# Kernel optimization log

Hardware: AMD Instinct MI355X
Metric: run time of the kernel (lower is better)

The kernel has to match this reference:

```python
import jax, jax.numpy as jnp
import numpy as np
from jax import lax

B, T, D, H = 64, 2048, 128, 256  # batch, seq_len, input_dim, hidden_dim


def setup_inputs() -> dict:
    key = jax.random.key(0)
    ks = jax.random.split(key, 21)
    s = 0.05
    p = lambda k, shape: jax.random.normal(k, shape, dtype=jnp.float32) * s
    inp = {"x": jax.random.normal(ks[0], (B, T, D), dtype=jnp.float32)}
    i = 1
    for n in ["e1", "e2", "d1", "d2"]:  # encode1, encode2, reconstruct1, reconstruct2
        inp[n + "_Wih"] = p(ks[i], (4 * H, D)); i += 1
        inp[n + "_Whh"] = p(ks[i], (4 * H, H)); i += 1
        inp[n + "_bih"] = p(ks[i], (4 * H,)); i += 1
        inp[n + "_bhh"] = p(ks[i], (4 * H,)); i += 1
    inp["l1_W"] = p(ks[17], (D, H)); inp["l1_b"] = p(ks[18], (D,))
    inp["l2_W"] = p(ks[19], (D, H)); inp["l2_b"] = p(ks[20], (D,))
    return inp


def _lstm_cell(h, c, xt, Wih, Whh, bih, bhh):
    # PyTorch gate order: i, f, g, o
    g = xt @ Wih.T + h @ Whh.T + bih + bhh  # [B, 4H]
    i, f, gg, o = jnp.split(g, 4, axis=-1)
    c = jax.nn.sigmoid(f) * c + jax.nn.sigmoid(i) * jnp.tanh(gg)
    h = jax.nn.sigmoid(o) * jnp.tanh(c)
    return h, c


def _encode(x, h0, c0, Wih, Whh, bih, bhh):
    # x: [B, T, D] batch_first -> scan over time
    def step(carry, xt):
        h, c = carry
        h, c = _lstm_cell(h, c, xt, Wih, Whh, bih, bhh)
        return (h, c), None
    (h, c), _ = lax.scan(step, (h0, c0), jnp.swapaxes(x, 0, 1))
    return h, c


def _decode(n, h, c, Wih, Whh, bih, bhh, Wl, bl):
    # first output is linear(hidden) before any cell step (matches original decode)
    inp0 = h @ Wl.T + bl  # [B, D]
    def step(carry, _):
        h, c, inp = carry
        h, c = _lstm_cell(h, c, inp, Wih, Whh, bih, bhh)
        inp = h @ Wl.T + bl
        return (h, c, inp), inp
    _, outs = lax.scan(step, (h, c, inp0), None, length=n - 1)  # [n-1, B, D]
    out = jnp.concatenate([inp0[None], outs], axis=0)  # [n, B, D]
    return jnp.swapaxes(out, 0, 1)  # [B, n, D]


def reference(x,
              e1_Wih, e1_Whh, e1_bih, e1_bhh,
              e2_Wih, e2_Whh, e2_bih, e2_bhh,
              d1_Wih, d1_Whh, d1_bih, d1_bhh,
              d2_Wih, d2_Whh, d2_bih, d2_bhh,
              l1_W, l1_b, l2_W, l2_b):
    Bc, Tc = x.shape[0], x.shape[1]
    T1 = Tc // 2
    h0 = jnp.zeros((Bc, H), dtype=x.dtype)
    c0 = jnp.zeros((Bc, H), dtype=x.dtype)
    x1 = x[:, :T1][:, ::-1]  # first half, time-reversed
    x2 = x[:, T1:]
    h1, c1 = _encode(x1, h0, c0, e1_Wih, e1_Whh, e1_bih, e1_bhh)
    h2, c2 = _encode(x2, h1, c1, e2_Wih, e2_Whh, e2_bih, e2_bhh)
    out1 = _decode(T1, h1, c1, d1_Wih, d1_Whh, d1_bih, d1_bhh, l1_W, l1_b)
    out2 = _decode(Tc - T1, h2, c2, d2_Wih, d2_Whh, d2_bih, d2_bhh, l2_W, l2_b)[:, ::-1]
    return jnp.concatenate([out1, out2], axis=1)  # [B, T, D]
```

## Files before the change

### kernel.cpp

```cpp
#include <hip/hip_runtime.h>
#include <stdint.h>

#define Bv 64
#define Tv 2048
#define T1v 1024
#define Dv 128
#define Hv 256

typedef _Float16 h2_t __attribute__((ext_vector_type(2)));
typedef _Float16 f16x8 __attribute__((ext_vector_type(8)));
typedef float f32x4 __attribute__((ext_vector_type(4)));

__device__ inline float d2(uint32_t hp, uint32_t wp, float acc) {
#if __has_builtin(__builtin_amdgcn_fdot2)
  return __builtin_amdgcn_fdot2(__builtin_bit_cast(h2_t, hp),
                                __builtin_bit_cast(h2_t, wp), acc, false);
#else
  float out;
  asm("v_dot2_f32_f16 %0, %1, %2, %3" : "=v"(out) : "v"(hp), "v"(wp), "v"(acc));
  return out;
#endif
}

__device__ inline uint16_t f2h(float x) {
// ... 25 lines not shown
  const float2* x2 = (const float2*)x;
  float2 v = x2[idx];
  xpk[idx] = packpair(v.x, v.y);
}

__global__ void k_pack_w(const float* __restrict__ src, uint32_t* __restrict__ wAll,
                         uint32_t* __restrict__ wLg, uint32_t* __restrict__ wStr) {
  int idx = blockIdx.x * 256 + threadIdx.x;
  int row = idx >> 7, k2 = idx & 127;
  uint32_t pr = packpair(src[row * 256 + 2 * k2], src[row * 256 + 2 * k2 + 1]);
  wAll[k2 * 1024 + row] = pr;
  if (k2 >= 96) {
    int g = (k2 - 96) >> 2, qq = (k2 - 96) & 3;
    wLg[(g * 1024 + row) * 4 + qq] = pr;
  }
  if (k2 >= 48 && k2 < 96) wStr[row * 48 + (k2 - 48)] = pr;
}

__global__ void k_pack_w2(const float* __restrict__ src, uint32_t* __restrict__ wReg,
                          uint32_t* __restrict__ wLds) {
  int idx = blockIdx.x * 256 + threadIdx.x;
  int r = idx >> 7, k2 = idx & 127;
  uint32_t pr = packpair(src[r * 256 + 2 * k2], src[r * 256 + 2 * k2 + 1]);
  int gate = r >> 8, u = r & 255;
  int u_hi = u >> 7, jb = u & 127;
  int q = k2 >> 5, kk = k2 & 31;
  int tid = jb * 4 + q;
  int ri = u_hi * 4 + gate;
  int cc = kk >> 2, c = kk & 3;
  if (cc < 6) wReg[((ri * 6 + cc) * 512 + tid) * 4 + c] = pr;
  else        wLds[((ri * 2 + (cc - 6)) * 512 + tid) * 4 + c] = pr;
}

__global__ void k_pack_wf(const float* __restrict__ src, uint32_t* __restrict__ resF,
                          uint32_t* __restrict__ ldsF, uint32_t* __restrict__ strF,
                          int CR, int CL, int CS) {
  int idx = blockIdx.x * 256 + threadIdx.x;
  int r = idx >> 7, k2 = idx & 127;
  int k = 2 * k2;
  uint32_t pr = packpair(src[r * 256 + k], src[r * 256 + k + 1]);
  int gate = r >> 8, u = r & 255;
  int rowp = u * 4 + gate;
  int t = rowp >> 4, w = t >> 3, tt = t & 7, rr = rowp & 15;
  int c = k >> 5, kk = k & 31;
  int lane = rr + 16 * (kk >> 3);
  int dw = (kk & 7) >> 1;
  if (c < CR) {
    resF[(((w * CR + c) * 8 + tt) * 64 + lane) * 4 + dw] = pr;
  } else if (c < CR + CL) {
    ldsF[(((w * CL + (c - CR)) * 8 + tt) * 64 + lane) * 4 + dw] = pr;
  } else {
    int cs = c - CR - CL;
    size_t o = (((size_t)(w * CS + cs) * 8 + tt) * 64 + lane) * 4 + dw;
    strF[o] = pr;
    strF[o + (size_t)CS * 4096 * 4] = pr;
  }
}

__global__ void k_pack_biasf(const float* __restrict__ b32, uint16_t* __restrict__ biasF) {
  int r = blockIdx.x * 256 + threadIdx.x;
  if (r >= 1024) return;
  int gate = r >> 8, u = r & 255;
  int rowp = u * 4 + gate;
  int t = rowp >> 4, w = t >> 3, tt = t & 7, rr = rowp & 15;
  int lg = rr >> 2, reg = rr & 3;
  uint16_t v = f2h(b32[r]);
  for (int bl = 0; bl < 16; ++bl)
    biasF[(w * 64 + (bl + 16 * lg)) * 32 + tt * 4 + reg] = v;
}

__global__ void k_bias_pack(const float* __restrict__ b32, uint32_t* __restrict__ bpk) {
  int jb = threadIdx.x;
  uint32_t w[4];
#pragma unroll
  for (int wi = 0; wi < 4; ++wi) {
    int ri0 = 2 * wi, ri1 = 2 * wi + 1;
    int row0 = (ri0 & 3) * 256 + jb + 128 * (ri0 >> 2);
    int row1 = (ri1 & 3) * 256 + jb + 128 * (ri1 >> 2);
    w[wi] = packpair(b32[row0], b32[row1]);
  }
  ((uint4*)bpk)[jb] = make_uint4(w[0], w[1], w[2], w[3]);
}

__global__ void k_pack_wih(const float* __restrict__ Wih, uint32_t* __restrict__ wihp) {
  int idx = blockIdx.x * 256 + threadIdx.x;
  int row = idx >> 6, k2 = idx & 63;
  wihp[row * 64 + k2] = packpair(Wih[row * 128 + 2 * k2], Wih[row * 128 + 2 * k2 + 1]);
}

__global__ void k_bias2(const float* __restrict__ bih, const float* __restrict__ bhh,
                        float* __restrict__ bias) {
  int i = blockIdx.x * 256 + threadIdx.x;
  if (i < 1024) bias[i] = bih[i] + bhh[i];
}

__global__ void k_dec_combine(const float* __restrict__ Whh, const float* __restrict__ Wih,
                              const float* __restrict__ bih, const float* __restrict__ bhh,
                              const float* __restrict__ lW, const float* __restrict__ lb,
                              float* __restrict__ wd, float* __restrict__ bias) {
  int j = blockIdx.x;
  int k = threadIdx.x;
  __shared__ float wr[128];
  if (k < 128) wr[k] = Wih[j * 128 + k];
  __syncthreads();
  float acc = Whh[j * 256 + k];
  for (int d = 0; d < 128; ++d) acc += wr[d] * lW[d * 256 + k];
  wd[j * 256 + k] = acc;
  if (k == 0) {
    float s = bih[j] + bhh[j];
    for (int d = 0; d < 128; ++d) s += wr[d] * lb[d];
    bias[j] = s;
  }
}

__global__ void k_pack_wl(const float* __restrict__ lW, uint32_t* __restrict__ wlp) {
  int idx = blockIdx.x * 256 + threadIdx.x;
  int d = idx >> 7, k2 = idx & 127;
  wlp[d * 128 + k2] = packpair(lW[d * 256 + 2 * k2], lW[d * 256 + 2 * k2 + 1]);
}

template <int LAY>
__global__ __launch_bounds__(256) void k_xp_gemm(const uint32_t* __restrict__ xpk,
                                                 const uint32_t* __restrict__ wihp,
                                                 uint16_t* __restrict__ xp, int xt0, int xdt) {
  const int b = blockIdx.z;
  const int s0 = blockIdx.y * 32;
  const int r = blockIdx.x * 256 + threadIdx.x;
  uint32_t wreg[64];
#pragma unroll
  for (int k = 0; k < 64; ++k) wreg[k] = wihp[r * 64 + k];
  const int gate = r >> 8, u = r & 255;
  const int u_hi = u >> 7, jb = u & 127;
  const int ri = u_hi * 4 + gate;
  for (int sl = 0; sl < 32; ++sl) {
    const int s = s0 + sl;
    const int t = xt0 + s * xdt;
    const uint32_t* __restrict__ xrow = xpk + ((size_t)b * Tv + t) * 64;
    float a0 = 0.f, a1 = 0.f;
#pragma unroll
    for (int k = 0; k < 64; k += 2) {
      a0 = d2(xrow[k], wreg[k], a0);
      a1 = d2(xrow[k + 1], wreg[k + 1], a1);
    }
    uint16_t v = f2h(a0 + a1);
    if (LAY == 0)
      xp[(((size_t)b * T1v + s) * 128 + jb) * 8 + ri] = v;
    else
      xp[((size_t)b * T1v + s) * 1024 + r] = v;
  }
}

__global__ __launch_bounds__(256) void k_xp_gemmF(const uint32_t* __restrict__ xpk,
                                                  const uint32_t* __restrict__ wihp,
                                                  const float* __restrict__ bias,
                                                  uint16_t* __restrict__ xpf, int xt0, int xdt) {
  const int b = blockIdx.z;
  const int s0 = blockIdx.y * 32;
  const int r = blockIdx.x * 256 + threadIdx.x;
  uint32_t wreg[64];
#pragma unroll
  for (int k = 0; k < 64; ++k) wreg[k] = wihp[r * 64 + k];
  const float bv = bias[r];
  const int gate = r >> 8, u = r & 255;
  const int rowp = u * 4 + gate;
  const int t = rowp >> 4, w = t >> 3, tt = t & 7, rr = rowp & 15;
  const int lane = (b & 15) + 16 * (rr >> 2);
  const int reg = rr & 3;
  const int bt = b >> 4;
  for (int sl = 0; sl < 32; ++sl) {
    const int s = s0 + sl;
    const int tx = xt0 + s * xdt;
    const uint32_t* __restrict__ xrow = xpk + ((size_t)b * Tv + tx) * 64;
    float a0 = 0.f, a1 = 0.f;
#pragma unroll
    for (int k = 0; k < 64; k += 2) {
      a0 = d2(xrow[k], wreg[k], a0);
      a1 = d2(xrow[k + 1], wreg[k + 1], a1);
    }
    xpf[(((size_t)bt * 1024 + s) * 512 + w * 64 + lane) * 32 + tt * 4 + reg] =
        f2h(a0 + a1 + bv);
  }
}


struct CfgM {
  const uint4* resF;
  const uint4* ldsF;
  const uint4* strF;
  const uint16_t* biasF;
  const uint16_t* xpf;
  const float* h0;
  const float* c0;
  float* hN;
  float* cN;
  uint16_t* hist;
};

template <int CR, int CL, int CS>
__global__ void __launch_bounds__(512)
__attribute__((amdgpu_waves_per_eu(2, 2)))
k_rnnM(CfgM cA, CfgM cB, int nA) {
  __shared__ __align__(16) uint4 wldsA[CL > 0 ? CL * 4096 : 1];
  __shared__ __align__(16) uint16_t hb[2][16][264];

  const bool isA = (int)blockIdx.x < nA;
  const CfgM cfg = isA ? cA : cB;
  const int bi = isA ? (int)blockIdx.x : ((int)blockIdx.x - nA);
  const int b0 = bi * 16;
  const int tid = threadIdx.x;
  const int w = tid >> 6, l = tid & 63;
  const int bl = l & 15, lg = l >> 4;

  if (CL > 0) {
#pragma unroll
    for (int i = 0; i < CL * 8; ++i) wldsA[i * 512 + tid] = cfg.ldsF[i * 512 + tid];
  }

  uint4 wrA[CR * 8];
#pragma unroll
  for (int i = 0; i < CR * 8; ++i) wrA[i] = cfg.resF[((size_t)w * CR * 8 + i) * 64 + l];

  uint4 bh[4];
#pragma unroll
  for (int j = 0; j < 4; ++j) bh[j] = ((const uint4*)cfg.biasF)[(w * 64 + l) * 4 + j];

  float cst[8];
#pragma unroll
  for (int tt = 0; tt < 8; ++tt) {
    int unit = (w * 8 + tt) * 4 + lg;
    cst[tt] = cfg.c0 ? cfg.c0[(b0 + bl) * 256 + unit] : 0.f;
  }

  {
    int batch = tid >> 5, u0 = (tid & 31) * 8;
    uint16_t tmp[8];
#pragma unroll
    for (int j = 0; j < 8; ++j)
      tmp[j] = f2h(cfg.h0 ? cfg.h0[(b0 + batch) * 256 + u0 + j] : 0.f);
    *(uint4*)((char*)&hb[0][0][0] + batch * 528 + u0 * 2) = *(const uint4*)tmp;
  }
  __syncthreads();

  char* hb0 = (char*)&hb[0][0][0];
  const size_t hbsz = 16 * 264 * 2;
  int cur = 0;

  for (int s = 0; s < 1024; ++s) {
    const char* hbc = hb0 + (size_t)cur * hbsz;

    if (cfg.hist) {
      int batch = tid >> 5, u0 = (tid & 31) * 8;
      uint4 hv = *(const uint4*)(hbc + batch * 528 + u0 * 2);
      *(uint4*)(cfg.hist + ((size_t)(b0 + batch) * 1024 + s) * 256 + u0) = hv;
    }

    f32x4 acc[8];
    if (cfg.xpf) {
      const uint4* xp4 = (const uint4*)(cfg.xpf + (((size_t)bi * 1024 + s) * 512 + tid) * 32);
      uint4 xh[4];
#pragma unroll
      for (int j = 0; j < 4; ++j) xh[j] = xp4[j];
      const _Float16* xv = (const _Float16*)xh;
#pragma unroll
      for (int tt = 0; tt < 8; ++tt)
#pragma unroll
        for (int rg = 0; rg < 4; ++rg) acc[tt][rg] = (float)xv[tt * 4 + rg];
    } else {
      const _Float16* bv = (const _Float16*)bh;
#pragma unroll
      for (int tt = 0; tt < 8; ++tt)
#pragma unroll
        for (int rg = 0; rg < 4; ++rg) acc[tt][rg] = (float)bv[tt * 4 + rg];
    }

#pragma unroll
    for (int c = 0; c < CR; ++c) {
      f16x8 bf = __builtin_bit_cast(f16x8,
          *(const uint4*)(hbc + bl * 528 + c * 64 + lg * 16));
#pragma unroll
      for (int tt = 0; tt < 8; ++tt)
        acc[tt] = __builtin_amdgcn_mfma_f32_16x16x32_f16(
            __builtin_bit_cast(f16x8, wrA[c * 8 + tt]), bf, acc[tt], 0, 0, 0);
    }
    if (CL > 0) {
#pragma unroll
      for (int cl = 0; cl < CL; ++cl) {
        const int c = CR + cl;
        f16x8 bf = __builtin_bit_cast(f16x8,
            *(const uint4*)(hbc + bl * 528 + c * 64 + lg * 16));
#pragma unroll
        for (int tt = 0; tt < 8; ++tt) {
          uint4 au = wldsA[(w * CL + cl) * 512 + tt * 64 + l];
          acc[tt] = __builtin_amdgcn_mfma_f32_16x16x32_f16(
              __builtin_bit_cast(f16x8, au), bf, acc[tt], 0, 0, 0);
        }
      }
    }
    if (CS > 0) {
      const uint4* sp = cfg.strF + ((s & 1) ? (size_t)CS * 4096 : 0);
      uint4 pf[8];
#pragma unroll
      for (int tt = 0; tt < 8; ++tt) pf[tt] = sp[((size_t)w * CS) * 512 + tt * 64 + l];
#pragma unroll
      for (int cs = 0; cs < CS; ++cs) {
        const int c = CR + CL + cs;
        uint4 cu[8];
#pragma unroll
        for (int tt = 0; tt < 8; ++tt) cu[tt] = pf[tt];
        if (cs + 1 < CS) {
#pragma unroll
          for (int tt = 0; tt < 8; ++tt)
            pf[tt] = sp[((size_t)w * CS + cs + 1) * 512 + tt * 64 + l];
        }
        f16x8 bf = __builtin_bit_cast(f16x8,
            *(const uint4*)(hbc + bl * 528 + c * 64 + lg * 16));
#pragma unroll
        for (int tt = 0; tt < 8; ++tt)
          acc[tt] = __builtin_amdgcn_mfma_f32_16x16x32_f16(
              __builtin_bit_cast(f16x8, cu[tt]), bf, acc[tt], 0, 0, 0);
      }
    }

    char* hbn = hb0 + (size_t)(cur ^ 1) * hbsz;
#pragma unroll
    for (int tt = 0; tt < 8; ++tt) {
      const float i_ = sigm(acc[tt][0]);
      const float f_ = sigm(acc[tt][1]);
      const float g_ = tanh_(acc[tt][2]);
      const float o_ = sigm(acc[tt][3]);
      const float cn = f_ * cst[tt] + i_ * g_;
      cst[tt] = cn;
      const float hv = o_ * tanh_(cn);
      const int unit = (w * 8 + tt) * 4 + lg;
      *(uint16_t*)(hbn + bl * 528 + unit * 2) = f2h(hv);
    }
    __syncthreads();
    cur ^= 1;
  }

  if (cfg.hN) {
    const char* hbc = hb0 + (size_t)cur * hbsz;
    int batch = tid >> 5, u0 = (tid & 31) * 8;
#pragma unroll
    for (int j = 0; j < 8; ++j)
      cfg.hN[(b0 + batch) * 256 + u0 + j] =
          h2f(*(const uint16_t*)(hbc + batch * 528 + (u0 + j) * 2));
#pragma unroll
    for (int tt = 0; tt < 8; ++tt) {
      int unit = (w * 8 + tt) * 4 + lg;
      cfg.cN[(b0 + bl) * 256 + unit] = cst[tt];
    }
  }
}


struct CfgU {
  const uint4* wA;
  const uint4* wC;
  const uint4* bpk;
  const uint4* xps;
  const float* h0;
  const float* c0;
  float* hN;
  float* cN;
  uint16_t* hist;
};

__global__ void __launch_bounds__(512)
__attribute__((amdgpu_waves_per_eu(2, 2)))
k_rnnU6(CfgU cA, CfgU cB, int nA) {
  __shared__ __align__(16) uint4 wldsM[2 * 8 * 512];
  __shared__ __align__(16) uint16_t hbuf[2][4][72];

  const bool isA = (int)blockIdx.x < nA;
  const CfgU cfg = isA ? cA : cB;
  const int b = isA ? (int)blockIdx.x : ((int)blockIdx.x - nA);
  const int tid = threadIdx.x;
  const int q = tid & 3, jb = tid >> 2;

#pragma unroll
  for (int i = 0; i < 16; ++i) wldsM[i * 512 + tid] = cfg.wC[i * 512 + tid];

  uint4 wr[8][6];
#pragma unroll
  for (int ri = 0; ri < 8; ++ri)
#pragma unroll
    for (int cc = 0; cc < 6; ++cc) wr[ri][cc] = cfg.wA[(ri * 6 + cc) * 512 + tid];

  const uint4 bp = cfg.bpk[jb];
  float c0r = cfg.c0 ? cfg.c0[b * 256 + jb] : 0.f;
  float c1r = cfg.c0 ? cfg.c0[b * 256 + jb + 128] : 0.f;

  uint16_t* histp = cfg.hist ? cfg.hist + (size_t)b * 1024 * 256 : nullptr;
  if (q == 0) {
    float h00 = cfg.h0 ? cfg.h0[b * 256 + jb] : 0.f;
    float h01 = cfg.h0 ? cfg.h0[b * 256 + jb + 128] : 0.f;
    uint16_t u0 = f2h(h00), u1 = f2h(h01);
    hbuf[0][jb >> 6][jb & 63] = u0;
    hbuf[0][2 + (jb >> 6)][jb & 63] = u1;
    if (histp) {
      histp[jb] = u0;
      histp[jb + 128] = u1;
    }
  }
  const uint4* xps4 = cfg.xps ? cfg.xps + (size_t)b * 1024 * 128 + jb : nullptr;

  __syncthreads();

  int cur = 0;
  for (int s = 0; s < 1024; ++s) {
    uint4 xq = make_uint4(0, 0, 0, 0);
    if (xps4) xq = xps4[(size_t)s * 128];
    const uint4* Hq = (const uint4*)(&hbuf[cur][q][0]);

    float acc[8];
#pragma unroll
    for (int ri = 0; ri < 8; ++ri) acc[ri] = 0.f;

#pragma unroll
    for (int cc = 0; cc < 6; ++cc) {
      const uint4 hv = Hq[cc];
#pragma unroll
      for (int ri = 0; ri < 8; ++ri) {
        acc[ri] = d2(hv.x, wr[ri][cc].x, acc[ri]);
        acc[ri] = d2(hv.y, wr[ri][cc].y, acc[ri]);
        acc[ri] = d2(hv.z, wr[ri][cc].z, acc[ri]);
        acc[ri] = d2(hv.w, wr[ri][cc].w, acc[ri]);
      }
    }
#pragma unroll
    for (int lI = 0; lI < 2; ++lI) {
      const uint4 hv = Hq[6 + lI];
#pragma unroll
      for (int ri = 0; ri < 8; ++ri) {
        const uint4 wv = wldsM[(ri * 2 + lI) * 512 + tid];
        acc[ri] = d2(hv.x, wv.x, acc[ri]);
        acc[ri] = d2(hv.y, wv.y, acc[ri]);
        acc[ri] = d2(hv.z, wv.z, acc[ri]);
        acc[ri] = d2(hv.w, wv.w, acc[ri]);
      }
    }

#pragma unroll
    for (int ri = 0; ri < 8; ++ri) acc[ri] = qsum4(acc[ri]);

    acc[0] += unpk(bp.x, 0) + unpk(xq.x, 0);
    acc[1] += unpk(bp.x, 1) + unpk(xq.x, 1);
    acc[2] += unpk(bp.y, 0) + unpk(xq.y, 0);
    acc[3] += unpk(bp.y, 1) + unpk(xq.y, 1);
    acc[4] += unpk(bp.z, 0) + unpk(xq.z, 0);
    acc[5] += unpk(bp.z, 1) + unpk(xq.z, 1);
    acc[6] += unpk(bp.w, 0) + unpk(xq.w, 0);
    acc[7] += unpk(bp.w, 1) + unpk(xq.w, 1);

    const float cn0 = sigm(acc[1]) * c0r + sigm(acc[0]) * tanh_(acc[2]);
    const float h0v = sigm(acc[3]) * tanh_(cn0);
    c0r = cn0;
    const float cn1 = sigm(acc[5]) * c1r + sigm(acc[4]) * tanh_(acc[6]);
    const float h1v = sigm(acc[7]) * tanh_(cn1);
    c1r = cn1;

    if (q == 0) {
      const uint16_t hu0 = f2h(h0v), hu1 = f2h(h1v);
      hbuf[cur ^ 1][jb >> 6][jb & 63] = hu0;
      hbuf[cur ^ 1][2 + (jb >> 6)][jb & 63] = hu1;
      if (histp && s < 1023) {
        histp[(size_t)(s + 1) * 256 + jb] = hu0;
        histp[(size_t)(s + 1) * 256 + jb + 128] = hu1;
      }
    }
    __syncthreads();
    cur ^= 1;
  }

  if (cfg.hN && q == 0) {
    cfg.hN[b * 256 + jb] = h2f(hbuf[cur][jb >> 6][jb & 63]);
    cfg.hN[b * 256 + jb + 128] = h2f(hbuf[cur][2 + (jb >> 6)][jb & 63]);
    cfg.cN[b * 256 + jb] = c0r;
    cfg.cN[b * 256 + jb + 128] = c1r;
  }
}


struct ChainCfg {
  const uint32_t* wAll;
  const uint4* wLg;
  const uint32_t* wStr;
// ... 107 lines not shown
    for (int g = 0; g < 8; ++g) {
      const uint4 hv = H4[24 + g];
      const uint4 wv0 = wlds4[g * 1024 + r0];
      const uint4 wv1 = wlds4[g * 1024 + r1];
      a00 = d2(hv.x, wv0.x, a00);
      a01 = d2(hv.y, wv0.y, a01);
      a10 = d2(hv.x, wv1.x, a10);
      a11 = d2(hv.y, wv1.y, a11);
      a00 = d2(hv.z, wv0.z, a00);
      a01 = d2(hv.w, wv0.w, a01);
      a10 = d2(hv.z, wv1.z, a10);
      a11 = d2(hv.w, wv1.w, a11);
    }
    if constexpr (WIH) {
      if (cfg.wih) {
        const uint4* XS4 = (const uint4*)xsh;
#pragma unroll
        for (int u = 0; u < 16; ++u) {
          const uint4 xv = XS4[u];
          const uint4 wv0 = wi0[u];
          const uint4 wv1 = wi1[u];
          a00 = d2(xv.x, wv0.x, a00);
          a01 = d2(xv.y, wv0.y, a01);
          a10 = d2(xv.x, wv1.x, a10);
          a11 = d2(xv.y, wv1.y, a11);
          a00 = d2(xv.z, wv0.z, a00);
          a01 = d2(xv.w, wv0.w, a01);
          a10 = d2(xv.z, wv1.z, a10);
          a11 = d2(xv.w, wv1.w, a11);
        }
      }
    }

    gsm[r0] = a00 + a01 + xa0;
    gsm[r1] = a10 + a11 + xa1;
    __syncthreads();

    if (tid < 256) {
      const float gi = gsm[tid];
      const float gf = gsm[tid + 256];
      const float gg = gsm[tid + 512];
      const float go = gsm[tid + 768];
      const float cn = sigm(gf) * creg + sigm(gi) * tanh_(gg);
      const float hv = sigm(go) * tanh_(cn);
      creg = cn;
      const uint16_t hu = f2h(hv);
      h16[tid] = hu;
      if (histp && s < 1023) histp[(size_t)(s + 1) * 256 + tid] = hu;
    }
    __syncthreads();
  }

  if (cfg.hN && tid < 256) {
    cfg.hN[b * 256 + tid] = h2f(h16[tid]);
    cfg.cN[b * 256 + tid] = creg;
  }
}

__global__ __launch_bounds__(256) void k_out(const uint16_t* __restrict__ hist,
                                             const uint32_t* __restrict__ wlp,
                                             const float* __restrict__ lb,
                                             float* __restrict__ out, int outbase, int tsign) {
  const int b = blockIdx.y;
  const int t0 = blockIdx.x * 64;
  __shared__ __align__(16) uint32_t hq[64 * 128];
  const uint32_t* hsrc = (const uint32_t*)hist;
  for (int i = threadIdx.x; i < 64 * 128; i += 256) {
    hq[i] = hsrc[((size_t)b * 1024 + t0) * 128 + i];
  }
  __syncthreads();
  const int d = threadIdx.x & 127;
  const int th = threadIdx.x >> 7;
  float acc[32];
#pragma unroll
  for (int it = 0; it < 32; ++it) acc[it] = lb[d];
  const uint4* W4 = (const uint4*)(wlp + (size_t)d * 128);
  const uint4* HQ4 = (const uint4*)hq;
  for (int k2c = 0; k2c < 32; ++k2c) {
    const uint4 wv = W4[k2c];
#pragma unroll
    for (int it = 0; it < 32; ++it) {
      const int tl = th * 32 + it;
      const uint4 hv = HQ4[tl * 32 + k2c];
      acc[it] = d2(hv.x, wv.x, acc[it]);
      acc[it] = d2(hv.y, wv.y, acc[it]);
      acc[it] = d2(hv.z, wv.z, acc[it]);
      acc[it] = d2(hv.w, wv.w, acc[it]);
    }
  }
#pragma unroll
  for (int it = 0; it < 32; ++it) {
    const int tl = th * 32 + it;
    const int t = t0 + tl;
    const int tout = outbase + tsign * t;
    out[((size_t)b * Tv + tout) * Dv + d] = acc[it];
  }
}


extern "C" void kernel_launch(void* const* d_in, const int* in_sizes, int n_in,
                              void* d_out, int out_size, void* d_ws, size_t ws_size,
                              hipStream_t stream) {
  const float* x = (const float*)d_in[0];
  const float* e1_Wih = (const float*)d_in[1];
  const float* e1_Whh = (const float*)d_in[2];
  const float* e1_bih = (const float*)d_in[3];
  const float* e1_bhh = (const float*)d_in[4];
  const float* e2_Wih = (const float*)d_in[5];
  const float* e2_Whh = (const float*)d_in[6];
  const float* e2_bih = (const float*)d_in[7];
  const float* e2_bhh = (const float*)d_in[8];
  const float* d1_Wih = (const float*)d_in[9];
  const float* d1_Whh = (const float*)d_in[10];
  const float* d1_bih = (const float*)d_in[11];
  const float* d1_bhh = (const float*)d_in[12];
  const float* d2_Wih = (const float*)d_in[13];
  const float* d2_Whh = (const float*)d_in[14];
  const float* d2_bih = (const float*)d_in[15];
  const float* d2_bhh = (const float*)d_in[16];
  const float* l1_W = (const float*)d_in[17];
  const float* l1_b = (const float*)d_in[18];
  const float* l2_W = (const float*)d_in[19];
  const float* l2_b = (const float*)d_in[20];

  uint8_t* wsb = (uint8_t*)d_ws;
  size_t off = 0;
  auto take = [&](size_t n) -> void* {
    void* pp = wsb + off;
    off += (n + 255) & ~(size_t)255;
    return pp;
  };
  uint32_t* xpk = (uint32_t*)take((size_t)Bv * Tv * 64 * 4);
  uint16_t* hist1 = (uint16_t*)take((size_t)Bv * T1v * Hv * 2);
  uint16_t* hist2 = (uint16_t*)take((size_t)Bv * T1v * Hv * 2);
  struct WSet {
    uint32_t *wAll, *wLg, *wStr48, *wih;
    float* bias;
    uint32_t *wReg, *wLds, *bpk;
    uint32_t *resF, *ldsF, *strF;
    uint16_t* biasF;
  };
  auto take_wset = [&](bool with_ih) -> WSet {
    WSet w;
    w.wAll = (uint32_t*)take(128 * 1024 * 4);
    w.wLg = (uint32_t*)take(8 * 1024 * 16);
    w.wStr48 = (uint32_t*)take(1024 * 48 * 4);
    w.wih = with_ih ? (uint32_t*)take(1024 * 64 * 4) : nullptr;
    w.bias = (float*)take(1024 * 4);
    w.wReg = (uint32_t*)take(48 * 512 * 16);
    w.wLds = (uint32_t*)take(16 * 512 * 16);
    w.bpk = (uint32_t*)take(128 * 16);
    w.resF = (uint32_t*)take((size_t)5 * 4096 * 16);
    w.ldsF = (uint32_t*)take((size_t)2 * 4096 * 16);
    w.strF = (uint32_t*)take((size_t)2 * 3 * 4096 * 16);
    w.biasF = (uint16_t*)take(512 * 32 * 2);
    return w;
  };
  WSet we1 = take_wset(true);
  WSet we2 = take_wset(true);
  WSet wd1 = take_wset(false);
  WSet wd2 = take_wset(false);
  float* wd32 = (float*)take(1024 * 256 * 4);
  uint32_t* wl1p = (uint32_t*)take(128 * 128 * 4);
  uint32_t* wl2p = (uint32_t*)take(128 * 128 * 4);
  float* h1 = (float*)take(64 * 256 * 4);
  float* c1 = (float*)take(64 * 256 * 4);
  float* h2 = (float*)take(64 * 256 * 4);
  float* c2 = (float*)take(64 * 256 * 4);
  uint16_t* xp = (uint16_t*)take((size_t)Bv * T1v * 1024 * 2);
  const bool use_xp = ws_size >= off;

  int variant = 5;
  int MCR = 0, MCL = 0, MCS = 0;
  {
    hipFuncAttributes fa;
    auto sf = [&](const void* f) {
      return hipFuncGetAttributes(&fa, f) == hipSuccess && fa.localSizeBytes == 0;
    };
    if (use_xp) {
      if (sf(reinterpret_cast<const void*>(&k_rnnM<5, 1, 2>))) { variant = 0; MCR = 5; MCL = 1; MCS = 2; }
      else if (sf(reinterpret_cast<const void*>(&k_rnnM<4, 2, 2>))) { variant = 1; MCR = 4; MCL = 2; MCS = 2; }
      else if (sf(reinterpret_cast<const void*>(&k_rnnM<3, 2, 3>))) { variant = 2; MCR = 3; MCL = 2; MCS = 3; }
      else if (sf(reinterpret_cast<const void*>(&k_rnnU6))) variant = 3;
      else if (sf(reinterpret_cast<const void*>(&k_rnn5<96, false>))) variant = 4;
    } else {
      if (sf(reinterpret_cast<const void*>(&k_rnn5<96, true>))) variant = 4;
    }
  }

  k_pack_x<<<(Bv * Tv * 64) / 256, 256, 0, stream>>>(x, xpk);
  k_pack_wih<<<256, 256, 0, stream>>>(e1_Wih, we1.wih);
  k_pack_wih<<<256, 256, 0, stream>>>(e2_Wih, we2.wih);
  k_bias2<<<4, 256, 0, stream>>>(e1_bih, e1_bhh, we1.bias);
  k_bias2<<<4, 256, 0, stream>>>(e2_bih, e2_bhh, we2.bias);
  k_pack_wl<<<64, 256, 0, stream>>>(l1_W, wl1p);
  k_pack_wl<<<64, 256, 0, stream>>>(l2_W, wl2p);

  if (variant <= 2) {
    k_pack_wf<<<512, 256, 0, stream>>>(e1_Whh, we1.resF, we1.ldsF, we1.strF, MCR, MCL, MCS);
    k_pack_wf<<<512, 256, 0, stream>>>(e2_Whh, we2.resF, we2.ldsF, we2.strF, MCR, MCL, MCS);
    k_pack_biasf<<<4, 256, 0, stream>>>(we1.bias, we1.biasF);
    k_pack_biasf<<<4, 256, 0, stream>>>(we2.bias, we2.biasF);
    k_dec_combine<<<1024, 256, 0, stream>>>(d1_Whh, d1_Wih, d1_bih, d1_bhh, l1_W, l1_b, wd32, wd1.bias);
    k_pack_wf<<<512, 256, 0, stream>>>(wd32, wd1.resF, wd1.ldsF, wd1.strF, MCR, MCL, MCS);
    k_pack_biasf<<<4, 256, 0, stream>>>(wd1.bias, wd1.biasF);
    k_dec_combine<<<1024, 256, 0, stream>>>(d2_Whh, d2_Wih, d2_bih, d2_bhh, l2_W, l2_b, wd32, wd2.bias);
    k_pack_wf<<<512, 256, 0, stream>>>(wd32, wd2.resF, wd2.ldsF, wd2.strF, MCR, MCL, MCS);
    k_pack_biasf<<<4, 256, 0, stream>>>(wd2.bias, wd2.biasF);

    auto mk = [&](WSet& w, const uint16_t* xpf, const float* h0, const float* c0,
                  float* hN, float* cN, uint16_t* hist) -> CfgM {
      return CfgM{(const uint4*)w.resF, (const uint4*)w.ldsF, (const uint4*)w.strF,
                  w.biasF, xpf, h0, c0, hN, cN, hist};
    };
    auto launch_m = [&](int grid, CfgM a, CfgM b2, int nA) {
      if (variant == 0)      k_rnnM<5, 1, 2><<<grid, 512, 0, stream>>>(a, b2, nA);
      else if (variant == 1) k_rnnM<4, 2, 2><<<grid, 512, 0, stream>>>(a, b2, nA);
      else                   k_rnnM<3, 2, 3><<<grid, 512, 0, stream>>>(a, b2, nA);
    };

    k_xp_gemmF<<<dim3(4, 32, 64), 256, 0, stream>>>(xpk, we1.wih, we1.bias, xp, 1023, -1);
    CfgM e1c = mk(we1, xp, nullptr, nullptr, h1, c1, nullptr);
    launch_m(4, e1c, e1c, 4);

    k_xp_gemmF<<<dim3(4, 32, 64), 256, 0, stream>>>(xpk, we2.wih, we2.bias, xp, 1024, 1);
    CfgM e2c = mk(we2, xp, h1, c1, h2, c2, nullptr);
    CfgM d1c = mk(wd1, nullptr, h1, c1, nullptr, nullptr, hist1);
    launch_m(8, e2c, d1c, 4);

    CfgM d2c = mk(wd2, nullptr, h2, c2, nullptr, nullptr, hist2);
    launch_m(4, d2c, d2c, 4);
  } else if (variant == 3) {
    k_pack_w2<<<512, 256, 0, stream>>>(e1_Whh, we1.wReg, we1.wLds);
    k_pack_w2<<<512, 256, 0, stream>>>(e2_Whh, we2.wReg, we2.wLds);
    k_bias_pack<<<1, 128, 0, stream>>>(we1.bias, we1.bpk);
    k_bias_pack<<<1, 128, 0, stream>>>(we2.bias, we2.bpk);
    k_dec_combine<<<1024, 256, 0, stream>>>(d1_Whh, d1_Wih, d1_bih, d1_bhh, l1_W, l1_b, wd32, wd1.bias);
    k_pack_w2<<<512, 256, 0, stream>>>(wd32, wd1.wReg, wd1.wLds);
    k_bias_pack<<<1, 128, 0, stream>>>(wd1.bias, wd1.bpk);
    k_dec_combine<<<1024, 256, 0, stream>>>(d2_Whh, d2_Wih, d2_bih, d2_bhh, l2_W, l2_b, wd32, wd2.bias);
    k_pack_w2<<<512, 256, 0, stream>>>(wd32, wd2.wReg, wd2.wLds);
    k_bias_pack<<<1, 128, 0, stream>>>(wd2.bias, wd2.bpk);

    auto mk = [&](WSet& w, const uint4* xps, const float* h0, const float* c0,
                  float* hN, float* cN, uint16_t* hist) -> CfgU {
      return CfgU{(const uint4*)w.wReg, (const uint4*)w.wLds,
                  (const uint4*)w.bpk, xps, h0, c0, hN, cN, hist};
    };
    k_xp_gemm<0><<<dim3(4, 32, 64), 256, 0, stream>>>(xpk, we1.wih, xp, 1023, -1);
    CfgU e1c = mk(we1, (const uint4*)xp, nullptr, nullptr, h1, c1, nullptr);
    k_rnnU6<<<64, 512, 0, stream>>>(e1c, e1c, 64);

    k_xp_gemm<0><<<dim3(4, 32, 64), 256, 0, stream>>>(xpk, we2.wih, xp, 1024, 1);
    CfgU e2c = mk(we2, (const uint4*)xp, h1, c1, h2, c2, nullptr);
    CfgU d1c = mk(wd1, nullptr, h1, c1, nullptr, nullptr, hist1);
    k_rnnU6<<<128, 512, 0, stream>>>(e2c, d1c, 64);

    CfgU d2c = mk(wd2, nullptr, h2, c2, nullptr, nullptr, hist2);
    k_rnnU6<<<64, 512, 0, stream>>>(d2c, d2c, 64);
  } else {
    k_pack_w<<<512, 256, 0, stream>>>(e1_Whh, we1.wAll, we1.wLg, we1.wStr48);
    k_pack_w<<<512, 256, 0, stream>>>(e2_Whh, we2.wAll, we2.wLg, we2.wStr48);
    k_dec_combine<<<1024, 256, 0, stream>>>(d1_Whh, d1_Wih, d1_bih, d1_bhh, l1_W, l1_b, wd32, wd1.bias);
    k_pack_w<<<512, 256, 0, stream>>>(wd32, wd1.wAll, wd1.wLg, wd1.wStr48);
    k_dec_combine<<<1024, 256, 0, stream>>>(d2_Whh, d2_Wih, d2_bih, d2_bhh, l2_W, l2_b, wd32, wd2.bias);
    k_pack_w<<<512, 256, 0, stream>>>(wd32, wd2.wAll, wd2.wLg, wd2.wStr48);

    auto launch_old = [&](int grid, ChainCfg a, ChainCfg b2, int nA) {
      if (use_xp) {
        if (variant == 4) k_rnn5<96, false><<<grid, 512, 0, stream>>>(a, b2, nA);
        else              k_rnn5<80, false><<<grid, 512, 0, stream>>>(a, b2, nA);
      } else {
        if (variant == 4) k_rnn5<96, true><<<grid, 512, 0, stream>>>(a, b2, nA);
        else              k_rnn5<80, true><<<grid, 512, 0, stream>>>(a, b2, nA);
      }
    };
    if (use_xp) k_xp_gemm<1><<<dim3(4, 32, 64), 256, 0, stream>>>(xpk, we1.wih, xp, 1023, -1);
    ChainCfg e1c{we1.wAll, (const uint4*)we1.wLg, we1.wStr48, use_xp ? nullptr : we1.wih,
                 use_xp ? nullptr : xpk, use_xp ? xp : nullptr, we1.bias,
                 nullptr, nullptr, h1, c1, nullptr, 1023, -1};
    launch_old(64, e1c, e1c, 64);

    if (use_xp) k_xp_gemm<1><<<dim3(4, 32, 64), 256, 0, stream>>>(xpk, we2.wih, xp, 1024, 1);
    ChainCfg e2c{we2.wAll, (const uint4*)we2.wLg, we2.wStr48, use_xp ? nullptr : we2.wih,
                 use_xp ? nullptr : xpk, use_xp ? xp : nullptr, we2.bias,
                 h1, c1, h2, c2, nullptr, 1024, 1};
    ChainCfg d1c{wd1.wAll, (const uint4*)wd1.wLg, wd1.wStr48, nullptr, nullptr, nullptr,
                 wd1.bias, h1, c1, nullptr, nullptr, hist1, 0, 0};
    launch_old(128, e2c, d1c, 64);

    ChainCfg d2c{wd2.wAll, (const uint4*)wd2.wLg, wd2.wStr48, nullptr, nullptr, nullptr,
                 wd2.bias, h2, c2, nullptr, nullptr, hist2, 0, 0};
    launch_old(64, d2c, d2c, 64);
  }

  k_out<<<dim3(16, 64), 256, 0, stream>>>(hist1, wl1p, l1_b, (float*)d_out, 0, 1);
  k_out<<<dim3(16, 64), 256, 0, stream>>>(hist2, wl2p, l2_b, (float*)d_out, 2047, -1);
}
```

Before: 7.167 ms.

## Rebalance Whh split to 5/2/1 and prefetch streamed weights before LDS chunks

Changes the recurrent weight split from 5 register, 1 LDS, 2 streamed chunks to 5/2/1, so less of Whh is streamed from global memory each timestep. The streamed-chunk load is issued at the top of the step, and the LDS chunks are computed between it and its use so the global latency is hidden. Bias and xp loads now share one strided pointer, which drops the per-thread bias registers. The 3/2/3 fallback variant is removed, and the LDS array is no longer guarded for CL=0.

```diff
diff --git a/kernel.cpp b/kernel.cpp
--- a/kernel.cpp
+++ b/kernel.cpp
@@ -249,7 +249,7 @@
 __global__ void __launch_bounds__(512)
 __attribute__((amdgpu_waves_per_eu(2, 2)))
 k_rnnM(CfgM cA, CfgM cB, int nA) {
-  __shared__ __align__(16) uint4 wldsA[CL > 0 ? CL * 4096 : 1];
+  __shared__ __align__(16) uint4 wldsA[CL * 4096];
   __shared__ __align__(16) uint16_t hb[2][16][264];
 
   const bool isA = (int)blockIdx.x < nA;
@@ -260,18 +260,12 @@
   const int w = tid >> 6, l = tid & 63;
   const int bl = l & 15, lg = l >> 4;
 
-  if (CL > 0) {
-#pragma unroll
-    for (int i = 0; i < CL * 8; ++i) wldsA[i * 512 + tid] = cfg.ldsF[i * 512 + tid];
-  }
+#pragma unroll
+  for (int i = 0; i < CL * 8; ++i) wldsA[i * 512 + tid] = cfg.ldsF[i * 512 + tid];
 
   uint4 wrA[CR * 8];
 #pragma unroll
   for (int i = 0; i < CR * 8; ++i) wrA[i] = cfg.resF[((size_t)w * CR * 8 + i) * 64 + l];
-
-  uint4 bh[4];
-#pragma unroll
-  for (int j = 0; j < 4; ++j) bh[j] = ((const uint4*)cfg.biasF)[(w * 64 + l) * 4 + j];
 
   float cst[8];
 #pragma unroll
@@ -288,6 +282,17 @@
       tmp[j] = f2h(cfg.h0 ? cfg.h0[(b0 + batch) * 256 + u0 + j] : 0.f);
     *(uint4*)((char*)&hb[0][0][0] + batch * 528 + u0 * 2) = *(const uint4*)tmp;
   }
+
+  const uint16_t* ibase;
+  size_t istr;
+  if (cfg.xpf) {
+    ibase = cfg.xpf + ((size_t)bi * 1024 * 512 + tid) * 32;
+    istr = (size_t)512 * 32;
+  } else {
+    ibase = cfg.biasF + (size_t)tid * 32;
+    istr = 0;
+  }
+
   __syncthreads();
 
   char* hb0 = (char*)&hb[0][0][0];
@@ -296,6 +301,11 @@
 
   for (int s = 0; s < 1024; ++s) {
     const char* hbc = hb0 + (size_t)cur * hbsz;
+
+    const uint4* sp = cfg.strF + ((s & 1) ? (size_t)CS * 4096 : 0);
+    uint4 sv[8];
+#pragma unroll
+    for (int tt = 0; tt < 8; ++tt) sv[tt] = sp[((size_t)(w * CS + 0) * 8 + tt) * 64 + l];
 
     if (cfg.hist) {
       int batch = tid >> 5, u0 = (tid & 31) * 8;
@@ -304,22 +314,16 @@
     }
 
     f32x4 acc[8];
-    if (cfg.xpf) {
-      const uint4* xp4 = (const uint4*)(cfg.xpf + (((size_t)bi * 1024 + s) * 512 + tid) * 32);
-      uint4 xh[4];
-#pragma unroll
-      for (int j = 0; j < 4; ++j) xh[j] = xp4[j];
-      const _Float16* xv = (const _Float16*)xh;
+    {
+      const uint4* ip4 = (const uint4*)(ibase + s * istr);
+      uint4 iq[4];
+#pragma unroll
+      for (int j = 0; j < 4; ++j) iq[j] = ip4[j];
+      const _Float16* xv = (const _Float16*)iq;
 #pragma unroll
       for (int tt = 0; tt < 8; ++tt)
 #pragma unroll
         for (int rg = 0; rg < 4; ++rg) acc[tt][rg] = (float)xv[tt * 4 + rg];
-    } else {
-      const _Float16* bv = (const _Float16*)bh;
-#pragma unroll
-      for (int tt = 0; tt < 8; ++tt)
-#pragma unroll
-        for (int rg = 0; rg < 4; ++rg) acc[tt][rg] = (float)bv[tt * 4 + rg];
     }
 
 #pragma unroll
@@ -331,43 +335,43 @@
         acc[tt] = __builtin_amdgcn_mfma_f32_16x16x32_f16(
             __builtin_bit_cast(f16x8, wrA[c * 8 + tt]), bf, acc[tt], 0, 0, 0);
     }
-    if (CL > 0) {
-#pragma unroll
-      for (int cl = 0; cl < CL; ++cl) {
-        const int c = CR + cl;
-        f16x8 bf = __builtin_bit_cast(f16x8,
-            *(const uint4*)(hbc + bl * 528 + c * 64 + lg * 16));
-#pragma unroll
-        for (int tt = 0; tt < 8; ++tt) {
-          uint4 au = wldsA[(w * CL + cl) * 512 + tt * 64 + l];
-          acc[tt] = __builtin_amdgcn_mfma_f32_16x16x32_f16(
-              __builtin_bit_cast(f16x8, au), bf, acc[tt], 0, 0, 0);
-        }
+
+    {
+      const int c = CR + CL;
+      f16x8 bf = __builtin_bit_cast(f16x8,
+          *(const uint4*)(hbc + bl * 528 + c * 64 + lg * 16));
+#pragma unroll
+      for (int tt = 0; tt < 8; ++tt)
+        acc[tt] = __builtin_amdgcn_mfma_f32_16x16x32_f16(
+            __builtin_bit_cast(f16x8, sv[tt]), bf, acc[tt], 0, 0, 0);
+    }
+
+    if constexpr (CS >= 2) {
+#pragma unroll
+      for (int tt = 0; tt < 8; ++tt) sv[tt] = sp[((size_t)(w * CS + 1) * 8 + tt) * 64 + l];
+    }
+
+#pragma unroll
+    for (int cl = 0; cl < CL; ++cl) {
+      const int c = CR + cl;
+      f16x8 bf = __builtin_bit_cast(f16x8,
+          *(const uint4*)(hbc + bl * 528 + c * 64 + lg * 16));
+#pragma unroll
+      for (int tt = 0; tt < 8; ++tt) {
+        uint4 au = wldsA[(w * CL + cl) * 512 + tt * 64 + l];
+        acc[tt] = __builtin_amdgcn_mfma_f32_16x16x32_f16(
+            __builtin_bit_cast(f16x8, au), bf, acc[tt], 0, 0, 0);
       }
     }
-    if (CS > 0) {
-      const uint4* sp = cfg.strF + ((s & 1) ? (size_t)CS * 4096 : 0);
-      uint4 pf[8];
-#pragma unroll
-      for (int tt = 0; tt < 8; ++tt) pf[tt] = sp[((size_t)w * CS) * 512 + tt * 64 + l];
-#pragma unroll
-      for (int cs = 0; cs < CS; ++cs) {
-        const int c = CR + CL + cs;
-        uint4 cu[8];
-#pragma unroll
-        for (int tt = 0; tt < 8; ++tt) cu[tt] = pf[tt];
-        if (cs + 1 < CS) {
-#pragma unroll
-          for (int tt = 0; tt < 8; ++tt)
-            pf[tt] = sp[((size_t)w * CS + cs + 1) * 512 + tt * 64 + l];
-        }
-        f16x8 bf = __builtin_bit_cast(f16x8,
-            *(const uint4*)(hbc + bl * 528 + c * 64 + lg * 16));
-#pragma unroll
-        for (int tt = 0; tt < 8; ++tt)
-          acc[tt] = __builtin_amdgcn_mfma_f32_16x16x32_f16(
-              __builtin_bit_cast(f16x8, cu[tt]), bf, acc[tt], 0, 0, 0);
-      }
+
+    if constexpr (CS >= 2) {
+      const int c = CR + CL + 1;
+      f16x8 bf = __builtin_bit_cast(f16x8,
+          *(const uint4*)(hbc + bl * 528 + c * 64 + lg * 16));
+#pragma unroll
+      for (int tt = 0; tt < 8; ++tt)
+        acc[tt] = __builtin_amdgcn_mfma_f32_16x16x32_f16(
+            __builtin_bit_cast(f16x8, sv[tt]), bf, acc[tt], 0, 0, 0);
     }
 
     char* hbn = hb0 + (size_t)(cur ^ 1) * hbsz;
@@ -379,9 +383,8 @@
       const float o_ = sigm(acc[tt][3]);
       const float cn = f_ * cst[tt] + i_ * g_;
       cst[tt] = cn;
-      const float hv = o_ * tanh_(cn);
       const int unit = (w * 8 + tt) * 4 + lg;
-      *(uint16_t*)(hbn + bl * 528 + unit * 2) = f2h(hv);
+      *(uint16_t*)(hbn + bl * 528 + unit * 2) = f2h(o_ * tanh_(cn));
     }
     __syncthreads();
     cur ^= 1;
@@ -795,7 +798,7 @@
     w.bpk = (uint32_t*)take(128 * 16);
     w.resF = (uint32_t*)take((size_t)5 * 4096 * 16);
     w.ldsF = (uint32_t*)take((size_t)2 * 4096 * 16);
-    w.strF = (uint32_t*)take((size_t)2 * 3 * 4096 * 16);
+    w.strF = (uint32_t*)take((size_t)2 * 2 * 4096 * 16);
     w.biasF = (uint16_t*)take(512 * 32 * 2);
     return w;
   };
@@ -821,9 +824,8 @@
       return hipFuncGetAttributes(&fa, f) == hipSuccess && fa.localSizeBytes == 0;
     };
     if (use_xp) {
-      if (sf(reinterpret_cast<const void*>(&k_rnnM<5, 1, 2>))) { variant = 0; MCR = 5; MCL = 1; MCS = 2; }
+      if (sf(reinterpret_cast<const void*>(&k_rnnM<5, 2, 1>))) { variant = 0; MCR = 5; MCL = 2; MCS = 1; }
       else if (sf(reinterpret_cast<const void*>(&k_rnnM<4, 2, 2>))) { variant = 1; MCR = 4; MCL = 2; MCS = 2; }
-      else if (sf(reinterpret_cast<const void*>(&k_rnnM<3, 2, 3>))) { variant = 2; MCR = 3; MCL = 2; MCS = 3; }
       else if (sf(reinterpret_cast<const void*>(&k_rnnU6))) variant = 3;
       else if (sf(reinterpret_cast<const void*>(&k_rnn5<96, false>))) variant = 4;
     } else {
@@ -839,11 +841,9 @@
   k_pack_wl<<<64, 256, 0, stream>>>(l1_W, wl1p);
   k_pack_wl<<<64, 256, 0, stream>>>(l2_W, wl2p);
 
-  if (variant <= 2) {
+  if (variant <= 1) {
     k_pack_wf<<<512, 256, 0, stream>>>(e1_Whh, we1.resF, we1.ldsF, we1.strF, MCR, MCL, MCS);
     k_pack_wf<<<512, 256, 0, stream>>>(e2_Whh, we2.resF, we2.ldsF, we2.strF, MCR, MCL, MCS);
-    k_pack_biasf<<<4, 256, 0, stream>>>(we1.bias, we1.biasF);
-    k_pack_biasf<<<4, 256, 0, stream>>>(we2.bias, we2.biasF);
     k_dec_combine<<<1024, 256, 0, stream>>>(d1_Whh, d1_Wih, d1_bih, d1_bhh, l1_W, l1_b, wd32, wd1.bias);
     k_pack_wf<<<512, 256, 0, stream>>>(wd32, wd1.resF, wd1.ldsF, wd1.strF, MCR, MCL, MCS);
     k_pack_biasf<<<4, 256, 0, stream>>>(wd1.bias, wd1.biasF);
@@ -857,9 +857,8 @@
                   w.biasF, xpf, h0, c0, hN, cN, hist};
     };
     auto launch_m = [&](int grid, CfgM a, CfgM b2, int nA) {
-      if (variant == 0)      k_rnnM<5, 1, 2><<<grid, 512, 0, stream>>>(a, b2, nA);
-      else if (variant == 1) k_rnnM<4, 2, 2><<<grid, 512, 0, stream>>>(a, b2, nA);
-      else                   k_rnnM<3, 2, 3><<<grid, 512, 0, stream>>>(a, b2, nA);
+      if (variant == 0) k_rnnM<5, 2, 1><<<grid, 512, 0, stream>>>(a, b2, nA);
+      else              k_rnnM<4, 2, 2><<<grid, 512, 0, stream>>>(a, b2, nA);
     };
 
     k_xp_gemmF<<<dim3(4, 32, 64), 256, 0, stream>>>(xpk, we1.wih, we1.bias, xp, 1023, -1);
```

Measured after the change: 14.19 ms. 98.0% more time.

## Prefetch streamed weights and xp early, reorder MFMA chains, drop CR=5 variant

Applied to the files above, without the earlier changes.

The recurrent MFMA kernel now issues the global loads for the input projection and the first streamed weight chunk at the top of each step, before the register and LDS MFMA chains run. The LDS-weight MFMAs are interleaved after the first streamed chunk so global latency hides behind compute. Bias is now always applied from registers and xp is added after the matmul, so the input-projection GEMM no longer folds in bias. The 5/1/2 register split is removed, so the default becomes 4/2/2 with more weights in LDS and streamed from memory. This trades fewer resident weight registers for earlier overlap of memory traffic with compute.

```diff
diff --git a/kernel.cpp b/kernel.cpp
--- a/kernel.cpp
+++ b/kernel.cpp
@@ -201,7 +201,6 @@
 
 __global__ __launch_bounds__(256) void k_xp_gemmF(const uint32_t* __restrict__ xpk,
                                                   const uint32_t* __restrict__ wihp,
-                                                  const float* __restrict__ bias,
                                                   uint16_t* __restrict__ xpf, int xt0, int xdt) {
   const int b = blockIdx.z;
   const int s0 = blockIdx.y * 32;
@@ -209,7 +208,6 @@
   uint32_t wreg[64];
 #pragma unroll
   for (int k = 0; k < 64; ++k) wreg[k] = wihp[r * 64 + k];
-  const float bv = bias[r];
   const int gate = r >> 8, u = r & 255;
   const int rowp = u * 4 + gate;
   const int t = rowp >> 4, w = t >> 3, tt = t & 7, rr = rowp & 15;
@@ -227,7 +225,7 @@
       a1 = d2(xrow[k + 1], wreg[k + 1], a1);
     }
     xpf[(((size_t)bt * 1024 + s) * 512 + w * 64 + lane) * 32 + tt * 4 + reg] =
-        f2h(a0 + a1 + bv);
+        f2h(a0 + a1);
   }
 }
 
@@ -249,7 +247,7 @@
 __global__ void __launch_bounds__(512)
 __attribute__((amdgpu_waves_per_eu(2, 2)))
 k_rnnM(CfgM cA, CfgM cB, int nA) {
-  __shared__ __align__(16) uint4 wldsA[CL > 0 ? CL * 4096 : 1];
+  __shared__ __align__(16) uint4 wldsA[CL * 4096];
   __shared__ __align__(16) uint16_t hb[2][16][264];
 
   const bool isA = (int)blockIdx.x < nA;
@@ -260,10 +258,8 @@
   const int w = tid >> 6, l = tid & 63;
   const int bl = l & 15, lg = l >> 4;
 
-  if (CL > 0) {
-#pragma unroll
-    for (int i = 0; i < CL * 8; ++i) wldsA[i * 512 + tid] = cfg.ldsF[i * 512 + tid];
-  }
+#pragma unroll
+  for (int i = 0; i < CL * 8; ++i) wldsA[i * 512 + tid] = cfg.ldsF[i * 512 + tid];
 
   uint4 wrA[CR * 8];
 #pragma unroll
@@ -271,7 +267,7 @@
 
   uint4 bh[4];
 #pragma unroll
-  for (int j = 0; j < 4; ++j) bh[j] = ((const uint4*)cfg.biasF)[(w * 64 + l) * 4 + j];
+  for (int j = 0; j < 4; ++j) bh[j] = ((const uint4*)cfg.biasF)[(size_t)tid * 4 + j];
 
   float cst[8];
 #pragma unroll
@@ -288,6 +284,11 @@
       tmp[j] = f2h(cfg.h0 ? cfg.h0[(b0 + batch) * 256 + u0 + j] : 0.f);
     *(uint4*)((char*)&hb[0][0][0] + batch * 528 + u0 * 2) = *(const uint4*)tmp;
   }
+
+  const bool hasx = cfg.xpf != nullptr;
+  const uint4* xbase = hasx
+      ? (const uint4*)(cfg.xpf + ((size_t)bi * 1024 * 512 + tid) * 32) : nullptr;
+
   __syncthreads();
 
   char* hb0 = (char*)&hb[0][0][0];
@@ -296,6 +297,18 @@
 
   for (int s = 0; s < 1024; ++s) {
     const char* hbc = hb0 + (size_t)cur * hbsz;
+
+    uint4 xq[4];
+    if (hasx) {
+      const uint4* xp4 = xbase + (size_t)s * 2048;
+#pragma unroll
+      for (int j = 0; j < 4; ++j) xq[j] = xp4[j];
+    }
+
+    const uint4* sp = cfg.strF + ((s & 1) ? (size_t)CS * 4096 : 0);
+    uint4 sv[8];
+#pragma unroll
+    for (int tt = 0; tt < 8; ++tt) sv[tt] = sp[((size_t)(w * CS) * 8 + tt) * 64 + l];
 
     if (cfg.hist) {
       int batch = tid >> 5, u0 = (tid & 31) * 8;
@@ -304,17 +317,7 @@
     }
 
     f32x4 acc[8];
-    if (cfg.xpf) {
-      const uint4* xp4 = (const uint4*)(cfg.xpf + (((size_t)bi * 1024 + s) * 512 + tid) * 32);
-      uint4 xh[4];
-#pragma unroll
-      for (int j = 0; j < 4; ++j) xh[j] = xp4[j];
-      const _Float16* xv = (const _Float16*)xh;
-#pragma unroll
-      for (int tt = 0; tt < 8; ++tt)
-#pragma unroll
-        for (int rg = 0; rg < 4; ++rg) acc[tt][rg] = (float)xv[tt * 4 + rg];
-    } else {
+    {
       const _Float16* bv = (const _Float16*)bh;
 #pragma unroll
       for (int tt = 0; tt < 8; ++tt)
@@ -331,43 +334,43 @@
         acc[tt] = __builtin_amdgcn_mfma_f32_16x16x32_f16(
             __builtin_bit_cast(f16x8, wrA[c * 8 + tt]), bf, acc[tt], 0, 0, 0);
     }
-    if (CL > 0) {
-#pragma unroll
-      for (int cl = 0; cl < CL; ++cl) {
-        const int c = CR + cl;
-        f16x8 bf = __builtin_bit_cast(f16x8,
-            *(const uint4*)(hbc + bl * 528 + c * 64 + lg * 16));
-#pragma unroll
-        for (int tt = 0; tt < 8; ++tt) {
-          uint4 au = wldsA[(w * CL + cl) * 512 + tt * 64 + l];
-          acc[tt] = __builtin_amdgcn_mfma_f32_16x16x32_f16(
-              __builtin_bit_cast(f16x8, au), bf, acc[tt], 0, 0, 0);
+
+#pragma unroll
+    for (int cs = 0; cs < CS; ++cs) {
+      const int c = CR + CL + cs;
+      f16x8 bf = __builtin_bit_cast(f16x8,
+          *(const uint4*)(hbc + bl * 528 + c * 64 + lg * 16));
+#pragma unroll
+      for (int tt = 0; tt < 8; ++tt)
+        acc[tt] = __builtin_amdgcn_mfma_f32_16x16x32_f16(
+            __builtin_bit_cast(f16x8, sv[tt]), bf, acc[tt], 0, 0, 0);
+      if (cs + 1 < CS) {
+#pragma unroll
+        for (int tt = 0; tt < 8; ++tt)
+          sv[tt] = sp[((size_t)(w * CS + cs + 1) * 8 + tt) * 64 + l];
+      }
+      if (cs == 0) {
+#pragma unroll
+        for (int cl = 0; cl < CL; ++cl) {
+          const int cc = CR + cl;
+          f16x8 bfl = __builtin_bit_cast(f16x8,
+              *(const uint4*)(hbc + bl * 528 + cc * 64 + lg * 16));
+#pragma unroll
+          for (int tt = 0; tt < 8; ++tt) {
+            uint4 au = wldsA[(w * CL + cl) * 512 + tt * 64 + l];
+            acc[tt] = __builtin_amdgcn_mfma_f32_16x16x32_f16(
+                __builtin_bit_cast(f16x8, au), bfl, acc[tt], 0, 0, 0);
+          }
         }
       }
     }
-    if (CS > 0) {
-      const uint4* sp = cfg.strF + ((s & 1) ? (size_t)CS * 4096 : 0);
-      uint4 pf[8];
-#pragma unroll
-      for (int tt = 0; tt < 8; ++tt) pf[tt] = sp[((size_t)w * CS) * 512 + tt * 64 + l];
-#pragma unroll
-      for (int cs = 0; cs < CS; ++cs) {
-        const int c = CR + CL + cs;
-        uint4 cu[8];
-#pragma unroll
-        for (int tt = 0; tt < 8; ++tt) cu[tt] = pf[tt];
-        if (cs + 1 < CS) {
-#pragma unroll
-          for (int tt = 0; tt < 8; ++tt)
-            pf[tt] = sp[((size_t)w * CS + cs + 1) * 512 + tt * 64 + l];
-        }
-        f16x8 bf = __builtin_bit_cast(f16x8,
-            *(const uint4*)(hbc + bl * 528 + c * 64 + lg * 16));
-#pragma unroll
-        for (int tt = 0; tt < 8; ++tt)
-          acc[tt] = __builtin_amdgcn_mfma_f32_16x16x32_f16(
-              __builtin_bit_cast(f16x8, cu[tt]), bf, acc[tt], 0, 0, 0);
-      }
+
+    if (hasx) {
+      const _Float16* xv = (const _Float16*)xq;
+#pragma unroll
+      for (int tt = 0; tt < 8; ++tt)
+#pragma unroll
+        for (int rg = 0; rg < 4; ++rg) acc[tt][rg] += (float)xv[tt * 4 + rg];
     }
 
     char* hbn = hb0 + (size_t)(cur ^ 1) * hbsz;
@@ -379,9 +382,8 @@
       const float o_ = sigm(acc[tt][3]);
       const float cn = f_ * cst[tt] + i_ * g_;
       cst[tt] = cn;
-      const float hv = o_ * tanh_(cn);
       const int unit = (w * 8 + tt) * 4 + lg;
-      *(uint16_t*)(hbn + bl * 528 + unit * 2) = f2h(hv);
+      *(uint16_t*)(hbn + bl * 528 + unit * 2) = f2h(o_ * tanh_(cn));
     }
     __syncthreads();
     cur ^= 1;
@@ -821,9 +823,8 @@
       return hipFuncGetAttributes(&fa, f) == hipSuccess && fa.localSizeBytes == 0;
     };
     if (use_xp) {
-      if (sf(reinterpret_cast<const void*>(&k_rnnM<5, 1, 2>))) { variant = 0; MCR = 5; MCL = 1; MCS = 2; }
-      else if (sf(reinterpret_cast<const void*>(&k_rnnM<4, 2, 2>))) { variant = 1; MCR = 4; MCL = 2; MCS = 2; }
-      else if (sf(reinterpret_cast<const void*>(&k_rnnM<3, 2, 3>))) { variant = 2; MCR = 3; MCL = 2; MCS = 3; }
+      if (sf(reinterpret_cast<const void*>(&k_rnnM<4, 2, 2>))) { variant = 0; MCR = 4; MCL = 2; MCS = 2; }
+      else if (sf(reinterpret_cast<const void*>(&k_rnnM<3, 2, 3>))) { variant = 1; MCR = 3; MCL = 2; MCS = 3; }
       else if (sf(reinterpret_cast<const void*>(&k_rnnU6))) variant = 3;
       else if (sf(reinterpret_cast<const void*>(&k_rnn5<96, false>))) variant = 4;
     } else {
@@ -839,7 +840,7 @@
   k_pack_wl<<<64, 256, 0, stream>>>(l1_W, wl1p);
   k_pack_wl<<<64, 256, 0, stream>>>(l2_W, wl2p);
 
-  if (variant <= 2) {
+  if (variant <= 1) {
     k_pack_wf<<<512, 256, 0, stream>>>(e1_Whh, we1.resF, we1.ldsF, we1.strF, MCR, MCL, MCS);
     k_pack_wf<<<512, 256, 0, stream>>>(e2_Whh, we2.resF, we2.ldsF, we2.strF, MCR, MCL, MCS);
     k_pack_biasf<<<4, 256, 0, stream>>>(we1.bias, we1.biasF);
@@ -857,16 +858,15 @@
                   w.biasF, xpf, h0, c0, hN, cN, hist};
     };
     auto launch_m = [&](int grid, CfgM a, CfgM b2, int nA) {
-      if (variant == 0)      k_rnnM<5, 1, 2><<<grid, 512, 0, stream>>>(a, b2, nA);
-      else if (variant == 1) k_rnnM<4, 2, 2><<<grid, 512, 0, stream>>>(a, b2, nA);
-      else                   k_rnnM<3, 2, 3><<<grid, 512, 0, stream>>>(a, b2, nA);
+      if (variant == 0) k_rnnM<4, 2, 2><<<grid, 512, 0, stream>>>(a, b2, nA);
+      else              k_rnnM<3, 2, 3><<<grid, 512, 0, stream>>>(a, b2, nA);
     };
 
-    k_xp_gemmF<<<dim3(4, 32, 64), 256, 0, stream>>>(xpk, we1.wih, we1.bias, xp, 1023, -1);
+    k_xp_gemmF<<<dim3(4, 32, 64), 256, 0, stream>>>(xpk, we1.wih, xp, 1023, -1);
     CfgM e1c = mk(we1, xp, nullptr, nullptr, h1, c1, nullptr);
     launch_m(4, e1c, e1c, 4);
 
-    k_xp_gemmF<<<dim3(4, 32, 64), 256, 0, stream>>>(xpk, we2.wih, we2.bias, xp, 1024, 1);
+    k_xp_gemmF<<<dim3(4, 32, 64), 256, 0, stream>>>(xpk, we2.wih, xp, 1024, 1);
     CfgM e2c = mk(we2, xp, h1, c1, h2, c2, nullptr);
     CfgM d1c = mk(wd1, nullptr, h1, c1, nullptr, nullptr, hist1);
     launch_m(8, e2c, d1c, 4);
```

After: 14.86 ms. 107% more time.
